# Kernel tuning notes

Measured on AMD Instinct MI355X. Metric: run time of the kernel, lower is better.

The kernel has to match this reference:

```python
import jax, jax.numpy as jnp
import numpy as np

B, T, E, A = 4, 4096, 512, 64

def setup_inputs() -> dict:
    key = jax.random.key(0)
    k1, k2, k3, k4 = jax.random.split(key, 4)
    embedded = jax.random.normal(k1, (B, T, E), dtype=jnp.float32)
    # torch Linear(E, A, bias=False): weight [A, E], y = x @ W.T. Store as [E, A].
    s = 1.0 / np.sqrt(E)
    Wq = jax.random.uniform(k2, (E, A), dtype=jnp.float32, minval=-s, maxval=s)
    Wk = jax.random.uniform(k3, (E, A), dtype=jnp.float32, minval=-s, maxval=s)
    Wv = jax.random.uniform(k4, (E, A), dtype=jnp.float32, minval=-s, maxval=s)
    return {"embedded": embedded, "Wq": Wq, "Wk": Wk, "Wv": Wv}

def reference(embedded, Wq, Wk, Wv):
    Q = embedded @ Wq  # [B, T, A]
    K = embedded @ Wk
    V = embedded @ Wv
    A_dim = V.shape[-1]
    scores = jnp.einsum('btd,bsd->bts', Q, K) / jnp.sqrt(jnp.float32(A_dim))  # [B, T, T]
    Tlen = scores.shape[-1]
    causal = jnp.tril(jnp.ones((Tlen, Tlen), dtype=bool))
    scores = jnp.where(causal, scores, -jnp.inf)
    attn = jax.nn.softmax(scores, axis=-1)
    out = jnp.einsum('bts,bsd->btd', attn, V)  # [B, T, A]
    return jnp.round(out, 4)
```

## Files before the change

### kernel.cpp

```cpp
#include <hip/hip_runtime.h>

#define B_ 4
#define T_ 4096
#define E_ 512
#define A_ 64
#define SQSCALE 0.1803368801111204f

typedef __attribute__((ext_vector_type(8)))  short bf16x8;
typedef __attribute__((ext_vector_type(8)))  unsigned short ushort8;
typedef __attribute__((ext_vector_type(4)))  unsigned int   u32x4;
typedef __attribute__((ext_vector_type(4)))  float f32x4;
typedef __attribute__((ext_vector_type(16))) float f32x16;

__device__ __forceinline__ unsigned short f2bf(float x) {
    union { float f; unsigned int u; } v; v.f = x;
    unsigned int r = v.u + 0x7fffu + ((v.u >> 16) & 1u);
    return (unsigned short)(r >> 16);
}
__device__ __forceinline__ unsigned cvtpk(float a, float b) {
    unsigned r;
    asm("v_cvt_pk_bf16_f32 %0, %1, %2" : "=v"(r) : "v"(a), "v"(b));
    return r;
}
__device__ __forceinline__ void pls(unsigned &a, unsigned &b) {
    asm("v_permlane32_swap_b32 %0, %1" : "+v"(a), "+v"(b));
}

__global__ __launch_bounds__(256) void prep_w(
    const float* __restrict__ Wq, const float* __restrict__ Wk,
    const float* __restrict__ Wv, unsigned short* __restrict__ Wp)
{
    const int e = blockIdx.x * 256 + threadIdx.x;
    const int nt = e >> 10;
    const int ks = (e >> 6) & 15;
    const int l  = e & 63;
    const int col = nt * 16 + (l & 15);
    const int kb  = ks * 32 + (l >> 4) * 8;
    const float* W = (col < 64) ? Wq : ((col < 128) ? Wk : Wv);
    const int cc = col & 63;
    const float sc = (col < 64) ? SQSCALE : 1.f;
    union { unsigned short s[8]; ushort8 v; } u;
    #pragma unroll
    for (int j = 0; j < 8; ++j) u.s[j] = f2bf(W[(kb + j) * 64 + cc] * sc);
    *(ushort8*)&Wp[(size_t)e * 8] = u.v;
}

__global__ __launch_bounds__(512, 4) void qkv_proj_kernel(
    const float* __restrict__ emb, const unsigned short* __restrict__ Wp,
    unsigned short* __restrict__ Qo, unsigned short* __restrict__ Kp,
    unsigned short* __restrict__ Vp)
{
    __shared__ unsigned short at[32][536];
    __shared__ unsigned short kt[32][72];
    __shared__ unsigned short vt[64][40];
    const int tid = threadIdx.x;
    const long row0 = (long)blockIdx.x * 32;

    {
        const int r = tid >> 4, c16 = tid & 15;
        const float* __restrict__ src = emb + (row0 + r) * 512;
        #pragma unroll
        for (int j = 0; j < 4; ++j) {
            const int col = j * 128 + c16 * 8;
            const float4 x0 = *(const float4*)(src + col);
            const float4 x1 = *(const float4*)(src + col + 4);
            u32x4 p;
            p[0] = cvtpk(x0.x, x0.y); p[1] = cvtpk(x0.z, x0.w);
            p[2] = cvtpk(x1.x, x1.y); p[3] = cvtpk(x1.z, x1.w);
            *(u32x4*)&at[r][col] = p;
        }
    }
    __syncthreads();

    const int w = tid >> 6, lane = tid & 63;
    const int c = lane & 15, hi = lane >> 4;
    const int rg = w & 1, ng = w >> 1;

    f32x4 acc[3];
    #pragma unroll
    for (int j = 0; j < 3; ++j) acc[j] = (f32x4){0.f, 0.f, 0.f, 0.f};

    #pragma unroll
    for (int ks = 0; ks < 16; ++ks) {
        const bf16x8 af = *(const bf16x8*)&at[rg * 16 + c][ks * 32 + hi * 8];
        #pragma unroll
        for (int j = 0; j < 3; ++j) {
            const int nt = ng * 3 + j;
            const bf16x8 bf_ = *(const bf16x8*)&Wp[((size_t)(nt * 16 + ks) * 64 + lane) * 8];
            acc[j] = __builtin_amdgcn_mfma_f32_16x16x32_bf16(af, bf_, acc[j], 0, 0, 0);
        }
    }

    #pragma unroll
    for (int j = 0; j < 3; ++j) {
        const int nt = ng * 3 + j;
        #pragma unroll
        for (int r4 = 0; r4 < 4; ++r4) {
            const int rloc = rg * 16 + hi * 4 + r4;
            const unsigned short v = f2bf(acc[j][r4]);
            if (nt < 4)       Qo[(row0 + rloc) * 64 + nt * 16 + c] = v;
            else if (nt < 8)  kt[rloc][(nt - 4) * 16 + c] = v;
            else              vt[(nt - 8) * 16 + c][rloc] = v;
        }
    }
    __syncthreads();

    const int tloc = (int)(row0 & 4095);
    const long bb = row0 >> 12;
    const int ci  = tloc >> 6;
    const int f_  = (tloc >> 5) & 1;
    const int ks0 = (tloc >> 4) & 3;
    if (tid < 256) {
        const int kk = tid >> 6, l = tid & 63;
        const ushort8 val = *(const ushort8*)&kt[l & 31][kk * 16 + (l >> 5) * 8];
        *(ushort8*)&Kp[((((bb * 64 + ci) * 2 + f_) * 4 + kk) * 64 + l) * 8] = val;
    } else {
        const int e = tid - 256;
        const int ksl = e >> 7, ct = (e >> 6) & 1, l = e & 63;
        const ushort8 val = *(const ushort8*)&vt[ct * 32 + (l & 31)][ksl * 16 + (l >> 5) * 8];
        *(ushort8*)&Vp[((((bb * 64 + ci) * 4 + ks0 + ksl) * 2 + ct) * 64 + l) * 8] = val;
    }
}

__global__ __launch_bounds__(512, 2) void attn_kernel(
    const unsigned short* __restrict__ Q, const unsigned short* __restrict__ Kp,
    const unsigned short* __restrict__ Vp, float* __restrict__ out)
{
    __shared__ float accbuf[8][32][64];
    __shared__ float mbuf[8][32], lbuf[8][32];
    __shared__ float scb[8][32];

    const int tid = threadIdx.x, w = tid >> 6, lane = tid & 63;
    const int c = lane & 31, h = lane >> 5;
    const int b = blockIdx.x & 3;
    const int u = blockIdx.x >> 2;
    const int t = (u < 64) ? (127 - u) : (u - 64);
    const int qb = t << 5;

    const unsigned short* __restrict__ Qb  = Q  + ((long)b * T_ + qb) * 64;
    const unsigned short* __restrict__ Kpb = Kp + (size_t)b * 64 * 8 * 512;
    const unsigned short* __restrict__ Vpb = Vp + (size_t)b * 64 * 8 * 512;

    bf16x8 qf[4];
    #pragma unroll
    for (int kk = 0; kk < 4; ++kk)
        qf[kk] = *(const bf16x8*)&Qb[(long)c * 64 + kk * 16 + h * 8];

    f32x16 acc[2];
    #pragma unroll
    for (int ct = 0; ct < 2; ++ct)
        #pragma unroll
        for (int j = 0; j < 16; ++j) acc[ct][j] = 0.f;
    float m = -1e30f, l = 0.f;

    const int nc = ((qb + 31) >> 6) + 1;

    bf16x8 kf[2][4];
    {
        const size_t cp = (w < nc) ? w : (nc - 1);
        #pragma unroll
        for (int f = 0; f < 2; ++f)
            #pragma unroll
            for (int kk = 0; kk < 4; ++kk)
                kf[f][kk] = *(const bf16x8*)&Kpb[(((cp * 2 + f) * 4 + kk) * 64 + lane) * 8];
    }

    for (int ci = w; ci < nc; ci += 8) {
        const long s0 = (long)ci << 6;

        bf16x8 vf[4][2];
        #pragma unroll
        for (int ks = 0; ks < 4; ++ks)
            #pragma unroll
            for (int ct = 0; ct < 2; ++ct)
                vf[ks][ct] = *(const bf16x8*)&Vpb[((((size_t)ci * 4 + ks) * 2 + ct) * 64 + lane) * 8];

        f32x16 sf[2];
        #pragma unroll
        for (int f = 0; f < 2; ++f) {
            #pragma unroll
            for (int j = 0; j < 16; ++j) sf[f][j] = 0.f;
            #pragma unroll
            for (int kk = 0; kk < 4; ++kk)
                sf[f] = __builtin_amdgcn_mfma_f32_32x32x16_bf16(kf[f][kk], qf[kk], sf[f], 0, 0, 0);
        }

        bf16x8 kn[2][4];
        {
            const int cin = ci + 8;
            const size_t cp = (cin < nc) ? cin : (nc - 1);
            #pragma unroll
            for (int f = 0; f < 2; ++f)
                #pragma unroll
                for (int kk = 0; kk < 4; ++kk)
                    kn[f][kk] = *(const bf16x8*)&Kpb[(((cp * 2 + f) * 4 + kk) * 64 + lane) * 8];
        }

        if ((int)s0 + 63 > qb) {
            #pragma unroll
            for (int f = 0; f < 2; ++f)
                #pragma unroll
                for (int r = 0; r < 16; ++r) {
                    const int key = (int)s0 + f * 32 + ((r & 3) + 8 * (r >> 2)) + 4 * h;
                    if (key > qb + c) sf[f][r] = -1e30f;
                }
        }

        float pm = sf[0][0];
        #pragma unroll
        for (int f = 0; f < 2; ++f)
            #pragma unroll
            for (int r = 0; r < 16; ++r) pm = fmaxf(pm, sf[f][r]);
        pm = fmaxf(pm, __shfl_xor(pm, 32));

        float mn = m;
        if (__any(pm > m)) {
            mn = fmaxf(m, pm);
            const float sc = exp2f(m - mn);
            m = mn;
            l *= sc;
            if (h == 0) scb[w][c] = sc;
            asm volatile("s_waitcnt lgkmcnt(0)" ::: "memory");
            __builtin_amdgcn_sched_barrier(0);
            float scr[16];
            #pragma unroll
            for (int r = 0; r < 16; ++r)
                scr[r] = scb[w][((r & 3) + 8 * (r >> 2)) + 4 * h];
            #pragma unroll
            for (int ct = 0; ct < 2; ++ct)
                #pragma unroll
                for (int r = 0; r < 16; ++r) acc[ct][r] *= scr[r];
        }

        float rs = 0.f;
        #pragma unroll
        for (int f = 0; f < 2; ++f)
            #pragma unroll
            for (int r = 0; r < 16; ++r) {
                const float p = exp2f(sf[f][r] - mn);
                sf[f][r] = p;
                rs += p;
            }
        rs += __shfl_xor(rs, 32);
        l += rs;

        #pragma unroll
        for (int f = 0; f < 2; ++f) {
            unsigned w01 = cvtpk(sf[f][0], sf[f][1]);
            unsigned w23 = cvtpk(sf[f][2], sf[f][3]);
            unsigned w45 = cvtpk(sf[f][4], sf[f][5]);
            unsigned w67 = cvtpk(sf[f][6], sf[f][7]);
            pls(w01, w45); pls(w23, w67);
            union { unsigned uu[4]; bf16x8 v; } pa0, pa1;
            pa0.uu[0] = w01; pa0.uu[1] = w23; pa0.uu[2] = w45; pa0.uu[3] = w67;
            unsigned x01 = cvtpk(sf[f][8],  sf[f][9]);
            unsigned x23 = cvtpk(sf[f][10], sf[f][11]);
            unsigned x45 = cvtpk(sf[f][12], sf[f][13]);
            unsigned x67 = cvtpk(sf[f][14], sf[f][15]);
            pls(x01, x45); pls(x23, x67);
            pa1.uu[0] = x01; pa1.uu[1] = x23; pa1.uu[2] = x45; pa1.uu[3] = x67;
            #pragma unroll
            for (int ct = 0; ct < 2; ++ct) {
                acc[ct] = __builtin_amdgcn_mfma_f32_32x32x16_bf16(pa0.v, vf[2 * f][ct],     acc[ct], 0, 0, 0);
                acc[ct] = __builtin_amdgcn_mfma_f32_32x32x16_bf16(pa1.v, vf[2 * f + 1][ct], acc[ct], 0, 0, 0);
            }
        }

        #pragma unroll
        for (int f = 0; f < 2; ++f)
            #pragma unroll
            for (int kk = 0; kk < 4; ++kk) kf[f][kk] = kn[f][kk];
    }

    if (h == 0) { mbuf[w][c] = m; lbuf[w][c] = l; }
    #pragma unroll
    for (int ct = 0; ct < 2; ++ct)
        #pragma unroll
        for (int r = 0; r < 16; ++r)
            accbuf[w][((r & 3) + 8 * (r >> 2)) + 4 * h][ct * 32 + c] = acc[ct][r];
    __syncthreads();
    #pragma unroll
    for (int i = 0; i < 4; ++i) {
        const int e = tid + i * 512;
        const int q = e >> 6, d = e & 63;
        float ms = mbuf[0][q];
        #pragma unroll
        for (int wv = 1; wv < 8; ++wv) ms = fmaxf(ms, mbuf[wv][q]);
        float ls = 0.f, os = 0.f;
        #pragma unroll
        for (int wv = 0; wv < 8; ++wv) {
            const float e_ = exp2f(mbuf[wv][q] - ms);
            ls += lbuf[wv][q] * e_;
            os += accbuf[wv][q][d] * e_;
        }
        out[((long)b * T_ + qb + q) * 64 + d] = os / ls;
    }
}

extern "C" void kernel_launch(void* const* d_in, const int* in_sizes, int n_in,
                              void* d_out, int out_size, void* d_ws, size_t ws_size,
                              hipStream_t stream)
{
    const float* emb = (const float*)d_in[0];
    const float* Wq  = (const float*)d_in[1];
    const float* Wk  = (const float*)d_in[2];
    const float* Wv  = (const float*)d_in[3];
    float* out = (float*)d_out;

    unsigned short* Qs = (unsigned short*)d_ws;
    unsigned short* Kp = Qs + (size_t)B_ * T_ * A_;
    unsigned short* Vp = Kp + (size_t)B_ * T_ * A_;
    unsigned short* Wp = Vp + (size_t)B_ * T_ * A_;

    prep_w<<<dim3(48), dim3(256), 0, stream>>>(Wq, Wk, Wv, Wp);
    qkv_proj_kernel<<<dim3(512), dim3(512), 0, stream>>>(emb, Wp, Qs, Kp, Vp);
    attn_kernel<<<dim3(512), dim3(512), 0, stream>>>(Qs, Kp, Vp, out);
}
```

Before: 51.75 us.

## Halve projection block size with register-blocked rows and tree reductions in softmax

The QKV projection kernel now runs 256 threads per block. Each wave computes both 16-row groups, so every weight fragment loaded from global memory feeds two MFMAs and weight reads are halved. In the attention kernel, the row max and row-sum reductions are split into four independent accumulators, which shortens the serial dependency chains. The cost is more registers and fewer waves in the projection kernel, and float summation order changes slightly.

Result: slower. 54.46 us (+5.2%).

```diff
diff --git a/kernel.cpp b/kernel.cpp
--- a/kernel.cpp
+++ b/kernel.cpp
@@ -45,7 +45,7 @@
     *(ushort8*)&Wp[(size_t)e * 8] = u.v;
 }
 
-__global__ __launch_bounds__(512, 4) void qkv_proj_kernel(
+__global__ __launch_bounds__(256, 3) void qkv_proj_kernel(
     const float* __restrict__ emb, const unsigned short* __restrict__ Wp,
     unsigned short* __restrict__ Qo, unsigned short* __restrict__ Kp,
     unsigned short* __restrict__ Vp)
@@ -57,51 +57,61 @@
     const long row0 = (long)blockIdx.x * 32;
 
     {
-        const int r = tid >> 4, c16 = tid & 15;
+        const int r = tid >> 3, c8 = tid & 7;
         const float* __restrict__ src = emb + (row0 + r) * 512;
         #pragma unroll
         for (int j = 0; j < 4; ++j) {
-            const int col = j * 128 + c16 * 8;
+            const int col = j * 128 + c8 * 16;
             const float4 x0 = *(const float4*)(src + col);
             const float4 x1 = *(const float4*)(src + col + 4);
-            u32x4 p;
-            p[0] = cvtpk(x0.x, x0.y); p[1] = cvtpk(x0.z, x0.w);
-            p[2] = cvtpk(x1.x, x1.y); p[3] = cvtpk(x1.z, x1.w);
-            *(u32x4*)&at[r][col] = p;
+            const float4 x2 = *(const float4*)(src + col + 8);
+            const float4 x3 = *(const float4*)(src + col + 12);
+            u32x4 p0, p1;
+            p0[0] = cvtpk(x0.x, x0.y); p0[1] = cvtpk(x0.z, x0.w);
+            p0[2] = cvtpk(x1.x, x1.y); p0[3] = cvtpk(x1.z, x1.w);
+            p1[0] = cvtpk(x2.x, x2.y); p1[1] = cvtpk(x2.z, x2.w);
+            p1[2] = cvtpk(x3.x, x3.y); p1[3] = cvtpk(x3.z, x3.w);
+            *(u32x4*)&at[r][col]     = p0;
+            *(u32x4*)&at[r][col + 8] = p1;
         }
     }
     __syncthreads();
 
     const int w = tid >> 6, lane = tid & 63;
     const int c = lane & 15, hi = lane >> 4;
-    const int rg = w & 1, ng = w >> 1;
-
-    f32x4 acc[3];
-    #pragma unroll
-    for (int j = 0; j < 3; ++j) acc[j] = (f32x4){0.f, 0.f, 0.f, 0.f};
+
+    f32x4 acc[2][3];
+    #pragma unroll
+    for (int rg = 0; rg < 2; ++rg)
+        #pragma unroll
+        for (int j = 0; j < 3; ++j) acc[rg][j] = (f32x4){0.f, 0.f, 0.f, 0.f};
 
     #pragma unroll
     for (int ks = 0; ks < 16; ++ks) {
-        const bf16x8 af = *(const bf16x8*)&at[rg * 16 + c][ks * 32 + hi * 8];
+        const bf16x8 a0 = *(const bf16x8*)&at[c][ks * 32 + hi * 8];
+        const bf16x8 a1 = *(const bf16x8*)&at[16 + c][ks * 32 + hi * 8];
         #pragma unroll
         for (int j = 0; j < 3; ++j) {
-            const int nt = ng * 3 + j;
+            const int nt = w * 3 + j;
             const bf16x8 bf_ = *(const bf16x8*)&Wp[((size_t)(nt * 16 + ks) * 64 + lane) * 8];
-            acc[j] = __builtin_amdgcn_mfma_f32_16x16x32_bf16(af, bf_, acc[j], 0, 0, 0);
+            acc[0][j] = __builtin_amdgcn_mfma_f32_16x16x32_bf16(a0, bf_, acc[0][j], 0, 0, 0);
+            acc[1][j] = __builtin_amdgcn_mfma_f32_16x16x32_bf16(a1, bf_, acc[1][j], 0, 0, 0);
         }
     }
 
     #pragma unroll
     for (int j = 0; j < 3; ++j) {
-        const int nt = ng * 3 + j;
-        #pragma unroll
-        for (int r4 = 0; r4 < 4; ++r4) {
-            const int rloc = rg * 16 + hi * 4 + r4;
-            const unsigned short v = f2bf(acc[j][r4]);
-            if (nt < 4)       Qo[(row0 + rloc) * 64 + nt * 16 + c] = v;
-            else if (nt < 8)  kt[rloc][(nt - 4) * 16 + c] = v;
-            else              vt[(nt - 8) * 16 + c][rloc] = v;
-        }
+        const int nt = w * 3 + j;
+        #pragma unroll
+        for (int rg = 0; rg < 2; ++rg)
+            #pragma unroll
+            for (int r4 = 0; r4 < 4; ++r4) {
+                const int rloc = rg * 16 + hi * 4 + r4;
+                const unsigned short v = f2bf(acc[rg][j][r4]);
+                if (nt < 4)       Qo[(row0 + rloc) * 64 + nt * 16 + c] = v;
+                else if (nt < 8)  kt[rloc][(nt - 4) * 16 + c] = v;
+                else              vt[(nt - 8) * 16 + c][rloc] = v;
+            }
     }
     __syncthreads();
 
@@ -110,13 +120,13 @@
     const int ci  = tloc >> 6;
     const int f_  = (tloc >> 5) & 1;
     const int ks0 = (tloc >> 4) & 3;
-    if (tid < 256) {
+    {
         const int kk = tid >> 6, l = tid & 63;
         const ushort8 val = *(const ushort8*)&kt[l & 31][kk * 16 + (l >> 5) * 8];
         *(ushort8*)&Kp[((((bb * 64 + ci) * 2 + f_) * 4 + kk) * 64 + l) * 8] = val;
-    } else {
-        const int e = tid - 256;
-        const int ksl = e >> 7, ct = (e >> 6) & 1, l = e & 63;
+    }
+    {
+        const int ksl = tid >> 7, ct = (tid >> 6) & 1, l = tid & 63;
         const ushort8 val = *(const ushort8*)&vt[ct * 32 + (l & 31)][ksl * 16 + (l >> 5) * 8];
         *(ushort8*)&Vp[((((bb * 64 + ci) * 4 + ks0 + ksl) * 2 + ct) * 64 + l) * 8] = val;
     }
@@ -206,11 +216,18 @@
                 }
         }
 
-        float pm = sf[0][0];
-        #pragma unroll
-        for (int f = 0; f < 2; ++f)
-            #pragma unroll
-            for (int r = 0; r < 16; ++r) pm = fmaxf(pm, sf[f][r]);
+        float t0 = fmaxf(sf[0][0], sf[1][0]);
+        float t1 = fmaxf(sf[0][1], sf[1][1]);
+        float t2 = fmaxf(sf[0][2], sf[1][2]);
+        float t3 = fmaxf(sf[0][3], sf[1][3]);
+        #pragma unroll
+        for (int r = 4; r < 16; r += 4) {
+            t0 = fmaxf(t0, fmaxf(sf[0][r],     sf[1][r]));
+            t1 = fmaxf(t1, fmaxf(sf[0][r + 1], sf[1][r + 1]));
+            t2 = fmaxf(t2, fmaxf(sf[0][r + 2], sf[1][r + 2]));
+            t3 = fmaxf(t3, fmaxf(sf[0][r + 3], sf[1][r + 3]));
+        }
+        float pm = fmaxf(fmaxf(t0, t1), fmaxf(t2, t3));
         pm = fmaxf(pm, __shfl_xor(pm, 32));
 
         float mn = m;
@@ -232,15 +249,19 @@
                 for (int r = 0; r < 16; ++r) acc[ct][r] *= scr[r];
         }
 
-        float rs = 0.f;
+        float s0a = 0.f, s1a = 0.f, s2a = 0.f, s3a = 0.f;
         #pragma unroll
         for (int f = 0; f < 2; ++f)
             #pragma unroll
-            for (int r = 0; r < 16; ++r) {
-                const float p = exp2f(sf[f][r] - mn);
-                sf[f][r] = p;
-                rs += p;
+            for (int r = 0; r < 16; r += 4) {
+                float p0 = exp2f(sf[f][r] - mn);
+                float p1 = exp2f(sf[f][r + 1] - mn);
+                float p2 = exp2f(sf[f][r + 2] - mn);
+                float p3 = exp2f(sf[f][r + 3] - mn);
+                sf[f][r] = p0; sf[f][r + 1] = p1; sf[f][r + 2] = p2; sf[f][r + 3] = p3;
+                s0a += p0; s1a += p1; s2a += p2; s3a += p3;
             }
+        float rs = (s0a + s1a) + (s2a + s3a);
         rs += __shfl_xor(rs, 32);
         l += rs;
 
@@ -313,6 +334,6 @@
     unsigned short* Wp = Vp + (size_t)B_ * T_ * A_;
 
     prep_w<<<dim3(48), dim3(256), 0, stream>>>(Wq, Wk, Wv, Wp);
-    qkv_proj_kernel<<<dim3(512), dim3(512), 0, stream>>>(emb, Wp, Qs, Kp, Vp);
+    qkv_proj_kernel<<<dim3(512), dim3(256), 0, stream>>>(emb, Wp, Qs, Kp, Vp);
     attn_kernel<<<dim3(512), dim3(512), 0, stream>>>(Qs, Kp, Vp, out);
 }
```

## Add MFMA priority hints, ILP reductions, unroll, and transposed padded accbuf

Applied to the files above, without the earlier changes.

Wraps the QK and PV MFMA sequences in s_setprio so the matrix wave gets issue priority, and unrolls the chunk loop by 2. The serial max and sum reductions are split into four independent chains to shorten dependency latency. The LDS accumulator buffer is transposed to [d][q] with padding to 34 and written with float2 stores, aiming to cut bank conflicts and store count in the epilogue. Unrolling raises register pressure under launch_bounds(512,2), which may cause spills.

Result: slower. 53.79 us (+3.9%).

```diff
diff --git a/kernel.cpp b/kernel.cpp
--- a/kernel.cpp
+++ b/kernel.cpp
@@ -126,7 +126,7 @@
     const unsigned short* __restrict__ Q, const unsigned short* __restrict__ Kp,
     const unsigned short* __restrict__ Vp, float* __restrict__ out)
 {
-    __shared__ float accbuf[8][32][64];
+    __shared__ float accbuf[8][64][34];
     __shared__ float mbuf[8][32], lbuf[8][32];
     __shared__ float scb[8][32];
 
@@ -165,6 +165,7 @@
                 kf[f][kk] = *(const bf16x8*)&Kpb[(((cp * 2 + f) * 4 + kk) * 64 + lane) * 8];
     }
 
+    #pragma unroll 2
     for (int ci = w; ci < nc; ci += 8) {
         const long s0 = (long)ci << 6;
 
@@ -177,13 +178,16 @@
 
         f32x16 sf[2];
         #pragma unroll
-        for (int f = 0; f < 2; ++f) {
+        for (int f = 0; f < 2; ++f)
             #pragma unroll
             for (int j = 0; j < 16; ++j) sf[f][j] = 0.f;
+        __builtin_amdgcn_s_setprio(1);
+        #pragma unroll
+        for (int f = 0; f < 2; ++f)
             #pragma unroll
             for (int kk = 0; kk < 4; ++kk)
                 sf[f] = __builtin_amdgcn_mfma_f32_32x32x16_bf16(kf[f][kk], qf[kk], sf[f], 0, 0, 0);
-        }
+        __builtin_amdgcn_s_setprio(0);
 
         bf16x8 kn[2][4];
         {
@@ -206,11 +210,18 @@
                 }
         }
 
-        float pm = sf[0][0];
-        #pragma unroll
-        for (int f = 0; f < 2; ++f)
-            #pragma unroll
-            for (int r = 0; r < 16; ++r) pm = fmaxf(pm, sf[f][r]);
+        float t0 = fmaxf(sf[0][0], sf[1][0]);
+        float t1 = fmaxf(sf[0][1], sf[1][1]);
+        float t2 = fmaxf(sf[0][2], sf[1][2]);
+        float t3 = fmaxf(sf[0][3], sf[1][3]);
+        #pragma unroll
+        for (int r = 4; r < 16; r += 4) {
+            t0 = fmaxf(t0, fmaxf(sf[0][r],     sf[1][r]));
+            t1 = fmaxf(t1, fmaxf(sf[0][r + 1], sf[1][r + 1]));
+            t2 = fmaxf(t2, fmaxf(sf[0][r + 2], sf[1][r + 2]));
+            t3 = fmaxf(t3, fmaxf(sf[0][r + 3], sf[1][r + 3]));
+        }
+        float pm = fmaxf(fmaxf(t0, t1), fmaxf(t2, t3));
         pm = fmaxf(pm, __shfl_xor(pm, 32));
 
         float mn = m;
@@ -232,15 +243,19 @@
                 for (int r = 0; r < 16; ++r) acc[ct][r] *= scr[r];
         }
 
-        float rs = 0.f;
-        #pragma unroll
-        for (int f = 0; f < 2; ++f)
-            #pragma unroll
-            for (int r = 0; r < 16; ++r) {
-                const float p = exp2f(sf[f][r] - mn);
-                sf[f][r] = p;
-                rs += p;
+        float s0a = 0.f, s1a = 0.f, s2a = 0.f, s3a = 0.f;
+        #pragma unroll
+        for (int f = 0; f < 2; ++f)
+            #pragma unroll
+            for (int r = 0; r < 16; r += 4) {
+                float p0 = exp2f(sf[f][r] - mn);
+                float p1 = exp2f(sf[f][r + 1] - mn);
+                float p2 = exp2f(sf[f][r + 2] - mn);
+                float p3 = exp2f(sf[f][r + 3] - mn);
+                sf[f][r] = p0; sf[f][r + 1] = p1; sf[f][r + 2] = p2; sf[f][r + 3] = p3;
+                s0a += p0; s1a += p1; s2a += p2; s3a += p3;
             }
+        float rs = (s0a + s1a) + (s2a + s3a);
         rs += __shfl_xor(rs, 32);
         l += rs;
 
@@ -259,11 +274,13 @@
             unsigned x67 = cvtpk(sf[f][14], sf[f][15]);
             pls(x01, x45); pls(x23, x67);
             pa1.uu[0] = x01; pa1.uu[1] = x23; pa1.uu[2] = x45; pa1.uu[3] = x67;
+            __builtin_amdgcn_s_setprio(1);
             #pragma unroll
             for (int ct = 0; ct < 2; ++ct) {
                 acc[ct] = __builtin_amdgcn_mfma_f32_32x32x16_bf16(pa0.v, vf[2 * f][ct],     acc[ct], 0, 0, 0);
                 acc[ct] = __builtin_amdgcn_mfma_f32_32x32x16_bf16(pa1.v, vf[2 * f + 1][ct], acc[ct], 0, 0, 0);
             }
+            __builtin_amdgcn_s_setprio(0);
         }
 
         #pragma unroll
@@ -276,8 +293,12 @@
     #pragma unroll
     for (int ct = 0; ct < 2; ++ct)
         #pragma unroll
-        for (int r = 0; r < 16; ++r)
-            accbuf[w][((r & 3) + 8 * (r >> 2)) + 4 * h][ct * 32 + c] = acc[ct][r];
+        for (int g = 0; g < 4; ++g) {
+            *(float2*)&accbuf[w][ct * 32 + c][g * 8 + 4 * h] =
+                make_float2(acc[ct][4 * g], acc[ct][4 * g + 1]);
+            *(float2*)&accbuf[w][ct * 32 + c][g * 8 + 4 * h + 2] =
+                make_float2(acc[ct][4 * g + 2], acc[ct][4 * g + 3]);
+        }
     __syncthreads();
     #pragma unroll
     for (int i = 0; i < 4; ++i) {
@@ -291,7 +312,7 @@
         for (int wv = 0; wv < 8; ++wv) {
             const float e_ = exp2f(mbuf[wv][q] - ms);
             ls += lbuf[wv][q] * e_;
-            os += accbuf[wv][q][d] * e_;
+            os += accbuf[wv][d][q] * e_;
         }
         out[((long)b * T_ + qb + q) * 64 + d] = os / ls;
     }
```
